# Kernel optimization log

Hardware: AMD Instinct MI355X
Metric: run time of the kernel (lower is better)

The kernel has to match this reference:

```python
import jax, jax.numpy as jnp
import numpy as np

C = 384       # in_channels
P = 64        # patch_size (H = W = P)
NH = 3        # num_heads
EPS = 1e-5
SCALE = (C // NH) ** -0.5  # head_dim in torch code = in_channels // num_heads


def _ln(x, w, b):
    m = jnp.mean(x, axis=-1, keepdims=True)
    v = jnp.var(x, axis=-1, keepdims=True)
    return (x - m) / jnp.sqrt(v + EPS) * w + b


def _dwt2d(x):
    # Haar DWT, x: [B, C, H, W] -> [B, 4C, H/2, W/2] channels = [LL, HL, LH, HH]
    x01 = x[:, :, 0::2, :] / 2
    x02 = x[:, :, 1::2, :] / 2
    x1 = x01[:, :, :, 0::2]
    x2 = x02[:, :, :, 0::2]
    x3 = x01[:, :, :, 1::2]
    x4 = x02[:, :, :, 1::2]
    return jnp.concatenate(
        [x1 + x2 + x3 + x4, -x1 - x2 + x3 + x4, -x1 + x2 - x3 + x4, x1 - x2 - x3 + x4],
        axis=1)


def _iwt2d(x):
    # inverse Haar, x: [B, 4C, h, w] -> [B, C, 2h, 2w]
    B, C4, h, w = x.shape
    c = C4 // 4
    x1 = x[:, 0:c] / 2
    x2 = x[:, c:2 * c] / 2
    x3 = x[:, 2 * c:3 * c] / 2
    x4 = x[:, 3 * c:4 * c] / 2
    out = jnp.zeros((B, c, h * 2, w * 2), x.dtype)
    out = out.at[:, :, 0::2, 0::2].set(x1 - x2 - x3 + x4)
    out = out.at[:, :, 1::2, 0::2].set(x1 - x2 + x3 - x4)
    out = out.at[:, :, 0::2, 1::2].set(x1 + x2 - x3 - x4)
    out = out.at[:, :, 1::2, 1::2].set(x1 + x2 + x3 + x4)
    return out


def setup_inputs():
    key = jax.random.key(0)
    ks = jax.random.split(key, 6)
    B, L = 8, P * P
    s = 0.02
    f32 = jnp.float32
    return {
        "sf": jax.random.normal(ks[0], (B, L, C), f32),
        "wf": jax.random.normal(ks[1], (B, L, C), f32),
        "q_w": jax.random.normal(ks[2], (C, C), f32) * s,
        "q_b": jnp.zeros((C,), f32),
        "q_ln_w": jnp.ones((C,), f32),
        "q_ln_b": jnp.zeros((C,), f32),
        "kv_w": jax.random.normal(ks[3], (2 * C, C), f32) * s,
        "kv_b": jnp.zeros((2 * C,), f32),
        "kv_ln_w": jnp.ones((2 * C,), f32),
        "kv_ln_b": jnp.zeros((2 * C,), f32),
        "out_w": jax.random.normal(ks[4], (C, C), f32) * s,
        "out_b": jnp.zeros((C,), f32),
    }


def reference(sf, wf, q_w, q_b, q_ln_w, q_ln_b, kv_w, kv_b, kv_ln_w, kv_ln_b, out_w, out_b):
    B, L, _ = sf.shape
    H = W = P
    h, w = H // 2, W // 2
    n = h * w  # L // 4

    t_sf = _ln(sf @ q_w.T + q_b, q_ln_w, q_ln_b)            # [B, L, C]
    t_wf = _ln(wf @ kv_w.T + kv_b, kv_ln_w, kv_ln_b)        # [B, L, 2C]

    t_sf = t_sf.reshape(B, H, W, C).transpose(0, 3, 1, 2)
    t_wf = t_wf.reshape(B, H, W, 2 * C).transpose(0, 3, 1, 2)

    t_sf = _dwt2d(t_sf).transpose(0, 2, 3, 1).reshape(B, n, 4 * C)
    t_wf = _dwt2d(t_wf).transpose(0, 2, 3, 1).reshape(B, n, 8 * C)

    k_all, v_all = jnp.split(t_wf, 2, axis=-1)              # each [B, n, 4C]
    q1, q2 = t_sf[..., :C], t_sf[..., C:]
    k1, k2 = k_all[..., :C], k_all[..., C:]
    v1, v2 = v_all[..., :C], v_all[..., C:]

    # branch 1: full single-head attention on LL sub-band (no scale, as in source)
    att1 = jax.nn.softmax(jnp.einsum('bnc,bmc->bnm', q1, k1), axis=-1)
    x1 = jnp.einsum('bnm,bmc->bnc', att1, v1)
    x1 = x1.reshape(B, h, w, C).transpose(0, 3, 1, 2)       # [B, C, h, w]

    # branch 2: multi-head attention on high-freq sub-bands, per-head dim = 3C/NH = C
    d = (3 * C) // NH
    q2 = q2.reshape(B, n, NH, d).transpose(0, 2, 1, 3)      # [B, NH, n, d]
    k2 = k2.reshape(B, n, NH, d).transpose(0, 2, 1, 3)
    v2 = v2.reshape(B, n, NH, d).transpose(0, 2, 3, 1)      # [B, NH, d, n]
    att2 = jax.nn.softmax(jnp.einsum('bhnd,bhmd->bhnm', q2, k2) * SCALE, axis=-1)
    x2 = jnp.einsum('bhdm,bhmn->bhdn', v2, att2)            # [B, NH, d, n]
    x2 = x2.reshape(B, NH * d, h, w)                        # [B, 3C, h, w]

    x = jnp.concatenate([x1, x2], axis=1)                   # [B, 4C, h, w]
    x = _iwt2d(x)                                           # [B, C, H, W]
    x = x.transpose(0, 2, 3, 1).reshape(B, L, C)
    return x @ out_w.T + out_b
```

## Files before the change

### kernel.cpp

```cpp
#include <hip/hip_runtime.h>
#include <hip/hip_bf16.h>

typedef unsigned short u16;
typedef unsigned int u32;
typedef __attribute__((ext_vector_type(8))) short short8;
typedef __attribute__((ext_vector_type(4))) float f32x4;

#define MFMA_BF16(A, B, C) __builtin_amdgcn_mfma_f32_16x16x32_bf16(A, B, C, 0, 0, 0)

#define SCALE2 0.08838834764831845f
#define LNEPS 1e-5f

__device__ __forceinline__ float b2f(u16 u) {
  return __uint_as_float(((u32)u) << 16);
}
__device__ __forceinline__ u16 f2b(float f) {
  u32 x = __float_as_uint(f);
  return (u16)((x + 0x7fffu + ((x >> 16) & 1u)) >> 16);
}
__device__ __forceinline__ float ldf(const float* p) { return *p; }
__device__ __forceinline__ float ldf(const u16* p) { return b2f(*p); }
__device__ __forceinline__ void stf(float* p, float v) { *p = v; }
__device__ __forceinline__ void stf(u16* p, float v) { *p = f2b(v); }

template <int SPLIT, typename TX, typename TO>
__global__ __launch_bounds__(256) void gemm_mfma(
    const TX* __restrict__ X, const float* __restrict__ W,
    const float* __restrict__ bias, TO* __restrict__ out) {
  __shared__ __align__(16) u16 AH[128 * 40];
  __shared__ __align__(16) u16 BH[128 * 40];
  __shared__ __align__(16) u16 AL[SPLIT ? 128 * 40 : 8];
  __shared__ __align__(16) u16 BL[SPLIT ? 128 * 40 : 8];
  const int tid = threadIdx.x;
  const int w = tid >> 6, lane = tid & 63;
  const int t = lane & 15, qd = lane >> 4;
  const int wm = w & 1, wn = w >> 1;
  const int m0 = blockIdx.y * 128, n0 = blockIdx.x * 128;
  f32x4 acc[4][4];
#pragma unroll
  for (int i = 0; i < 4; ++i)
#pragma unroll
    for (int j = 0; j < 4; ++j) acc[i][j] = (f32x4){0.f, 0.f, 0.f, 0.f};
  for (int kt = 0; kt < 384; kt += 32) {
#pragma unroll
    for (int rep = 0; rep < 4; ++rep) {
      int e = tid + rep * 256;
      int m = e >> 3, k4 = (e & 7) * 4;
      if constexpr (sizeof(TX) == 4) {
        float4 v = *(const float4*)(X + (size_t)(m0 + m) * 384 + kt + k4);
        u16 h0 = f2b(v.x), h1 = f2b(v.y), h2 = f2b(v.z), h3 = f2b(v.w);
        u32 hp0 = (u32)h0 | ((u32)h1 << 16), hp1 = (u32)h2 | ((u32)h3 << 16);
        *(uint2*)&AH[m * 40 + k4] = make_uint2(hp0, hp1);
        if (SPLIT) {
          u16 l0 = f2b(v.x - b2f(h0)), l1 = f2b(v.y - b2f(h1));
          u16 l2 = f2b(v.z - b2f(h2)), l3 = f2b(v.w - b2f(h3));
          *(uint2*)&AL[m * 40 + k4] =
              make_uint2((u32)l0 | ((u32)l1 << 16), (u32)l2 | ((u32)l3 << 16));
        }
      } else {
        uint2 raw = *(const uint2*)(X + (size_t)(m0 + m) * 384 + kt + k4);
        *(uint2*)&AH[m * 40 + k4] = raw;
      }
      float4 wv = *(const float4*)(W + (size_t)(n0 + m) * 384 + kt + k4);
      u16 wh0 = f2b(wv.x), wh1 = f2b(wv.y), wh2 = f2b(wv.z), wh3 = f2b(wv.w);
      *(uint2*)&BH[m * 40 + k4] =
          make_uint2((u32)wh0 | ((u32)wh1 << 16), (u32)wh2 | ((u32)wh3 << 16));
      if (SPLIT) {
        u16 wl0 = f2b(wv.x - b2f(wh0)), wl1 = f2b(wv.y - b2f(wh1));
        u16 wl2 = f2b(wv.z - b2f(wh2)), wl3 = f2b(wv.w - b2f(wh3));
        *(uint2*)&BL[m * 40 + k4] =
            make_uint2((u32)wl0 | ((u32)wl1 << 16), (u32)wl2 | ((u32)wl3 << 16));
      }
    }
    __syncthreads();
    short8 af[4], bf[4], al[4], bl[4];
#pragma unroll
    for (int mi = 0; mi < 4; ++mi) {
      af[mi] = *(const short8*)&AH[(wm * 64 + mi * 16 + t) * 40 + qd * 8];
      bf[mi] = *(const short8*)&BH[(wn * 64 + mi * 16 + t) * 40 + qd * 8];
      if (SPLIT) {
        al[mi] = *(const short8*)&AL[(wm * 64 + mi * 16 + t) * 40 + qd * 8];
        bl[mi] = *(const short8*)&BL[(wn * 64 + mi * 16 + t) * 40 + qd * 8];
      }
    }
#pragma unroll
    for (int mi = 0; mi < 4; ++mi)
#pragma unroll
      for (int ni = 0; ni < 4; ++ni) {
        acc[mi][ni] = MFMA_BF16(af[mi], bf[ni], acc[mi][ni]);
        if (SPLIT) {
          acc[mi][ni] = MFMA_BF16(al[mi], bf[ni], acc[mi][ni]);
          acc[mi][ni] = MFMA_BF16(af[mi], bl[ni], acc[mi][ni]);
        }
      }
    __syncthreads();
  }
#pragma unroll
  for (int ni = 0; ni < 4; ++ni) {
    int n = n0 + wn * 64 + ni * 16 + t;
    float bv = bias[n];
#pragma unroll
    for (int mi = 0; mi < 4; ++mi)
#pragma unroll
      for (int r = 0; r < 4; ++r) {
        int m = m0 + wm * 64 + mi * 16 + qd * 4 + r;
        stf(&out[(size_t)m * 384 + n], acc[mi][ni][r] + bv);
      }
  }
}

template <typename T>
__global__ __launch_bounds__(256) void ln_inplace(
    T* __restrict__ Tb, const float* __restrict__ w, const float* __restrict__ b, int N) {
  const int row = blockIdx.x, tid = threadIdx.x;
  T* Tr = Tb + (size_t)row * N;
  float vals[3];
  float s = 0.f, ss = 0.f;
  int nv = 0;
  for (int i = tid; i < N; i += 256) {
    float v = ldf(&Tr[i]);
    vals[nv++] = v;
    s += v; ss += v * v;
  }
#pragma unroll
  for (int mk = 32; mk; mk >>= 1) { s += __shfl_xor(s, mk); ss += __shfl_xor(ss, mk); }
  __shared__ float red[8];
  if ((tid & 63) == 0) { red[tid >> 6] = s; red[4 + (tid >> 6)] = ss; }
  __syncthreads();
  s = red[0] + red[1] + red[2] + red[3];
  ss = red[4] + red[5] + red[6] + red[7];
  float inv = 1.f / (float)N;
  float mean = s * inv;
  float var = fmaxf(ss * inv - mean * mean, 0.f);
  float rstd = rsqrtf(var + LNEPS);
  nv = 0;
  for (int i = tid; i < N; i += 256) {
    float v = (vals[nv++] - mean) * rstd * w[i] + b[i];
    stf(&Tr[i], v);
  }
}

__global__ __launch_bounds__(256) void ln_wf_split(
    float* __restrict__ lo, u16* __restrict__ hi,
    const float* __restrict__ w, const float* __restrict__ b) {
  const int row = blockIdx.x, tid = threadIdx.x;
  float* L = lo + (size_t)row * 384;
  u16* H = hi + (size_t)row * 384;
  float vals[3];
  float s = 0.f, ss = 0.f;
  int nv = 0;
  for (int i = tid; i < 768; i += 256) {
    float v = (i < 384) ? L[i] : b2f(H[i - 384]);
    vals[nv++] = v;
    s += v; ss += v * v;
  }
#pragma unroll
  for (int mk = 32; mk; mk >>= 1) { s += __shfl_xor(s, mk); ss += __shfl_xor(ss, mk); }
  __shared__ float red[8];
  if ((tid & 63) == 0) { red[tid >> 6] = s; red[4 + (tid >> 6)] = ss; }
  __syncthreads();
  s = red[0] + red[1] + red[2] + red[3];
  ss = red[4] + red[5] + red[6] + red[7];
  float mean = s * (1.f / 768.f);
  float var = fmaxf(ss * (1.f / 768.f) - mean * mean, 0.f);
  float rstd = rsqrtf(var + LNEPS);
  nv = 0;
  for (int i = 0 + tid; i < 768; i += 256) {
    float v = (vals[nv++] - mean) * rstd * w[i] + b[i];
    if (i < 384) L[i] = v; else H[i - 384] = f2b(v);
  }
}

__global__ __launch_bounds__(256) void dwt_sf(
    const float* __restrict__ T, u16* __restrict__ q1h, u16* __restrict__ q1l,
    u16* __restrict__ q2) {
  const int blk = blockIdx.x;
  const int b = blk >> 10, pos = blk & 1023;
  const int i = pos >> 5, j = pos & 31;
  const int p00 = (i * 2) * 64 + j * 2;
  const float* base = T + (size_t)b * 4096 * 384;
  for (int ch = threadIdx.x; ch < 384; ch += 256) {
    float a  = base[(size_t)p00 * 384 + ch];
    float cc = base[(size_t)(p00 + 1) * 384 + ch];
    float bb = base[(size_t)(p00 + 64) * 384 + ch];
    float dd = base[(size_t)(p00 + 65) * 384 + ch];
    float s0 = 0.5f * ( a + bb + cc + dd);
    float s1 = 0.5f * (-a - bb + cc + dd);
    float s2 = 0.5f * (-a + bb - cc + dd);
    float s3 = 0.5f * ( a - bb - cc + dd);
    size_t po = (size_t)(b * 1024 + pos) * 384 + ch;
    u16 h = f2b(s0);
    q1h[po] = h;
    q1l[po] = f2b(s0 - b2f(h));
    q2[(size_t)((b * 3 + 0) * 1024 + pos) * 384 + ch] = f2b(s1);
    q2[(size_t)((b * 3 + 1) * 1024 + pos) * 384 + ch] = f2b(s2);
    q2[(size_t)((b * 3 + 2) * 1024 + pos) * 384 + ch] = f2b(s3);
  }
}

__global__ __launch_bounds__(256) void dwt_wf_split(
    const float* __restrict__ lo, const u16* __restrict__ hi,
    u16* __restrict__ k1h, u16* __restrict__ k1l, u16* __restrict__ v1,
    u16* __restrict__ k2, u16* __restrict__ v2) {
  const int blk = blockIdx.x;
  const int b = blk >> 10, pos = blk & 1023;
  const int i = pos >> 5, j = pos & 31;
  const int p00 = (i * 2) * 64 + j * 2;
  for (int ch = threadIdx.x; ch < 768; ch += 256) {
    float a, bb, cc, dd;
    if (ch < 384) {
      const float* base = lo + (size_t)b * 4096 * 384;
      a  = base[(size_t)p00 * 384 + ch];
      cc = base[(size_t)(p00 + 1) * 384 + ch];
      bb = base[(size_t)(p00 + 64) * 384 + ch];
      dd = base[(size_t)(p00 + 65) * 384 + ch];
    } else {
      const u16* base = hi + (size_t)b * 4096 * 384;
      int c = ch - 384;
      a  = b2f(base[(size_t)p00 * 384 + c]);
      cc = b2f(base[(size_t)(p00 + 1) * 384 + c]);
      bb = b2f(base[(size_t)(p00 + 64) * 384 + c]);
      dd = b2f(base[(size_t)(p00 + 65) * 384 + c]);
    }
    float s0 = 0.5f * ( a + bb + cc + dd);
    float s1 = 0.5f * (-a - bb + cc + dd);
    float s2 = 0.5f * (-a + bb - cc + dd);
    float s3 = 0.5f * ( a - bb - cc + dd);
    if (ch < 384) {
      size_t po = (size_t)(b * 1024 + pos) * 384 + ch;
      u16 h = f2b(s0);
      k1h[po] = h;
      k1l[po] = f2b(s0 - b2f(h));
      v1[po] = f2b(s2);
      k2[(size_t)((b * 3 + 1) * 1024 + pos) * 384 + ch] = f2b(s1);
      v2[(size_t)((b * 3 + 1) * 1024 + pos) * 384 + ch] = f2b(s3);
    } else {
      int c = ch - 384;
      k2[(size_t)((b * 3 + 0) * 1024 + pos) * 384 + c] = f2b(s0);
      k2[(size_t)((b * 3 + 2) * 1024 + pos) * 384 + c] = f2b(s1);
      v2[(size_t)((b * 3 + 0) * 1024 + pos) * 384 + c] = f2b(s2);
      v2[(size_t)((b * 3 + 2) * 1024 + pos) * 384 + c] = f2b(s3);
    }
  }
}

__global__ __launch_bounds__(256) void transpose_rm(
    const u16* __restrict__ in, u16* __restrict__ out) {
  __shared__ u16 T[64][65];
  const int tid = threadIdx.x;
  const int bh = blockIdx.z, r0 = blockIdx.y * 64, c0 = blockIdx.x * 64;
  const u16* ip = in + ((size_t)bh * 1024 + r0) * 384 + c0;
  for (int i = tid; i < 2048; i += 256) {
    int r = i >> 5, c2 = i & 31;
    u32 v = *(const u32*)(ip + (size_t)r * 384 + c2 * 2);
    T[c2 * 2][r] = (u16)v;
    T[c2 * 2 + 1][r] = (u16)(v >> 16);
  }
  __syncthreads();
  u16* op = out + ((size_t)bh * 384 + c0) * 1024 + r0;
  for (int i = tid; i < 2048; i += 256) {
    int c = i >> 5, r2 = i & 31;
    u32 v = (u32)T[c][r2 * 2] | ((u32)T[c][r2 * 2 + 1] << 16);
    *(u32*)(op + (size_t)c * 1024 + r2 * 2) = v;
  }
}

__device__ __forceinline__ void xcd24v2(int L, int& bh, int& o0) {
  int s = L >> 3;
  bh = (s >> 4) * 8 + (L & 7);
  o0 = (s & 15) * 64;
}

__global__ __launch_bounds__(256) void att2_stats(
    const u16* __restrict__ q, const u16* __restrict__ k,
    float2* __restrict__ stats, float scale) {
  __shared__ __align__(16) u16 S[2][12 * 32 * 40];
  const int tid = threadIdx.x, w = tid >> 6, lane = tid & 63;
  const int t = lane & 15, qd = lane >> 4;
  int bh, o0;
  xcd24v2(blockIdx.x, bh, o0);
  short8 Ah[12];
  {
    const u16* qp = q + ((size_t)bh * 1024 + o0 + w * 16 + t) * 384 + qd * 8;
#pragma unroll
    for (int ks = 0; ks < 12; ++ks) Ah[ks] = *(const short8*)(qp + ks * 32);
  }
  float m[4] = {-1e30f, -1e30f, -1e30f, -1e30f}, l[4] = {0.f, 0.f, 0.f, 0.f};
  const u16* kb = k + (size_t)bh * 1024 * 384;
  int buf = 0;
  for (int st = 0; st < 32; ++st) {
#pragma unroll
    for (int i = 0; i < 6; ++i) {
      int u = tid + i * 256;
      int r = u / 48, c8 = u % 48;
      int ks = c8 >> 2, qq = c8 & 3;
      uint4 v = *(const uint4*)(kb + (size_t)(st * 32 + r) * 384 + c8 * 8);
      *(uint4*)&S[buf][(ks * 32 + r) * 40 + qq * 8] = v;
    }
    __syncthreads();
    f32x4 Sa0 = {0.f,0.f,0.f,0.f}, Sb0 = {0.f,0.f,0.f,0.f};
    f32x4 Sa1 = {0.f,0.f,0.f,0.f}, Sb1 = {0.f,0.f,0.f,0.f};
#pragma unroll
    for (int ks = 0; ks < 12; ks += 2) {
      short8 B00 = *(const short8*)&S[buf][(ks * 32 + t) * 40 + qd * 8];
      short8 B01 = *(const short8*)&S[buf][((ks + 1) * 32 + t) * 40 + qd * 8];
      short8 B10 = *(const short8*)&S[buf][(ks * 32 + 16 + t) * 40 + qd * 8];
      short8 B11 = *(const short8*)&S[buf][((ks + 1) * 32 + 16 + t) * 40 + qd * 8];
      Sa0 = MFMA_BF16(Ah[ks], B00, Sa0);
      Sb0 = MFMA_BF16(Ah[ks + 1], B01, Sb0);
      Sa1 = MFMA_BF16(Ah[ks], B10, Sa1);
      Sb1 = MFMA_BF16(Ah[ks + 1], B11, Sb1);
    }
#pragma unroll
    for (int r = 0; r < 4; ++r) {
      float s0 = (Sa0[r] + Sb0[r]) * scale;
      float s1 = (Sa1[r] + Sb1[r]) * scale;
      float mx = fmaxf(s0, s1);
#pragma unroll
      for (int mk = 1; mk < 16; mk <<= 1) mx = fmaxf(mx, __shfl_xor(mx, mk));
      float nm = fmaxf(m[r], mx);
      float e = __expf(s0 - nm) + __expf(s1 - nm);
#pragma unroll
      for (int mk = 1; mk < 16; mk <<= 1) e += __shfl_xor(e, mk);
      l[r] = l[r] * __expf(m[r] - nm) + e;
      m[r] = nm;
    }
    buf ^= 1;
  }
  if (t == 0) {
#pragma unroll
    for (int r = 0; r < 4; ++r)
      stats[(size_t)bh * 1024 + o0 + w * 16 + qd * 4 + r] =
          make_float2(m[r], 1.f / l[r]);
  }
}

__global__ __launch_bounds__(256, 2) void att2_accum(
    const u16* __restrict__ own, const u16* __restrict__ str,
    const u16* __restrict__ vt, const float2* __restrict__ stats,
    u16* __restrict__ xall, float scale) {
  __shared__ __align__(16) u16 SQ[12 * 32 * 40];
  __shared__ __align__(16) u16 SV[24 * 16 * 40];
  __shared__ __align__(16) u16 P[4][16 * 40];
  const int tid = threadIdx.x, w = tid >> 6, lane = tid & 63;
  const int t = lane & 15, qd = lane >> 4;
  int bh, o0;
  xcd24v2(blockIdx.x, bh, o0);
  short8 Ah[12];
  {
    const u16* op = own + ((size_t)bh * 1024 + o0 + w * 16 + t) * 384 + qd * 8;
#pragma unroll
    for (int ks = 0; ks < 12; ++ks) Ah[ks] = *(const short8*)(op + ks * 32);
  }
  f32x4 acc[24];
#pragma unroll
  for (int i = 0; i < 24; ++i) acc[i] = (f32x4){0.f, 0.f, 0.f, 0.f};
  const u16* sb = str + (size_t)bh * 1024 * 384;
  const u16* vb = vt + (size_t)bh * 384 * 1024;
  u16* Pw = &P[w][0];
  for (int st = 0; st < 32; ++st) {
    __syncthreads();
#pragma unroll
    for (int i = 0; i < 6; ++i) {
      int u = tid + i * 256;
      int r = u / 48, c8 = u % 48;
      int ks = c8 >> 2, qq = c8 & 3;
      uint4 v = *(const uint4*)(sb + (size_t)(st * 32 + r) * 384 + c8 * 8);
      *(uint4*)&SQ[(ks * 32 + r) * 40 + qq * 8] = v;
    }
#pragma unroll
    for (int i = 0; i < 6; ++i) {
      int u = tid + i * 256;
      int d = u >> 2, cq = u & 3;
      uint4 v = *(const uint4*)(vb + (size_t)d * 1024 + st * 32 + cq * 8);
      *(uint4*)&SV[d * 40 + cq * 8] = v;
    }
    float2 cs0 = stats[(size_t)bh * 1024 + st * 32 + t];
    float2 cs1 = stats[(size_t)bh * 1024 + st * 32 + 16 + t];
    __syncthreads();
    f32x4 Sa0 = {0.f,0.f,0.f,0.f}, Sb0 = {0.f,0.f,0.f,0.f};
    f32x4 Sa1 = {0.f,0.f,0.f,0.f}, Sb1 = {0.f,0.f,0.f,0.f};
#pragma unroll
    for (int ks = 0; ks < 12; ks += 2) {
      short8 B00 = *(const short8*)&SQ[(ks * 32 + t) * 40 + qd * 8];
      short8 B01 = *(const short8*)&SQ[((ks + 1) * 32 + t) * 40 + qd * 8];
      short8 B10 = *(const short8*)&SQ[(ks * 32 + 16 + t) * 40 + qd * 8];
      short8 B11 = *(const short8*)&SQ[((ks + 1) * 32 + 16 + t) * 40 + qd * 8];
      Sa0 = MFMA_BF16(Ah[ks], B00, Sa0);
      Sb0 = MFMA_BF16(Ah[ks + 1], B01, Sb0);
      Sa1 = MFMA_BF16(Ah[ks], B10, Sa1);
      Sb1 = MFMA_BF16(Ah[ks + 1], B11, Sb1);
    }
#pragma unroll
    for (int r = 0; r < 4; ++r) {
      float p0 = __expf((Sa0[r] + Sb0[r]) * scale - cs0.x) * cs0.y;
      float p1 = __expf((Sa1[r] + Sb1[r]) * scale - cs1.x) * cs1.y;
      Pw[(qd * 4 + r) * 40 + t] = f2b(p0);
      Pw[(qd * 4 + r) * 40 + 16 + t] = f2b(p1);
    }
    short8 Pa = *(const short8*)&Pw[t * 40 + qd * 8];
#pragma unroll
    for (int nj = 0; nj < 24; ++nj) {
      short8 Vf = *(const short8*)&SV[(nj * 16 + t) * 40 + qd * 8];
      acc[nj] = MFMA_BF16(Pa, Vf, acc[nj]);
    }
  }
  const int b_out = bh / 3, off = (1 + bh % 3) * 384;
#pragma unroll
  for (int nj = 0; nj < 24; ++nj)
#pragma unroll
    for (int r = 0; r < 4; ++r) {
      int row = o0 + w * 16 + qd * 4 + r;
      int d = nj * 16 + t;
      xall[((size_t)b_out * 1024 + row) * 1536 + off + d] = f2b(acc[nj][r]);
    }
}

__global__ __launch_bounds__(256, 2) void att1_fused(
    const u16* __restrict__ qh, const u16* __restrict__ ql,
    const u16* __restrict__ kh, const u16* __restrict__ kl,
    const u16* __restrict__ vt, float* __restrict__ part,
    float2* __restrict__ ml) {
  __shared__ __align__(16) u16 KH[12 * 1288];
  __shared__ __align__(16) u16 KL[12 * 1288];
  __shared__ __align__(16) u16 P[2][16 * 40];
  __shared__ float2 comb[2][2][16];
  const int tid = threadIdx.x, w = tid >> 6, lane = tid & 63;
  const int t = lane & 15, qd = lane >> 4;
  const int wr = w & 1, sh = w >> 1;
  const int bh = blockIdx.x & 7;
  const int q = blockIdx.x >> 3;
  const int o0 = (q & 31) * 32;
  const int sseg = q >> 5;
  const int sbase = sseg * 512;
  short8 Ah[12], Al[12];
  {
    const u16* qp  = qh + ((size_t)bh * 1024 + o0 + wr * 16 + t) * 384 + qd * 8;
    const u16* qp2 = ql + ((size_t)bh * 1024 + o0 + wr * 16 + t) * 384 + qd * 8;
#pragma unroll
    for (int ks = 0; ks < 12; ++ks) {
      Ah[ks] = *(const short8*)(qp + ks * 32);
      Al[ks] = *(const short8*)(qp2 + ks * 32);
    }
  }
  f32x4 acc[12];
#pragma unroll
  for (int i = 0; i < 12; ++i) acc[i] = (f32x4){0.f, 0.f, 0.f, 0.f};
  float m[4] = {-1e30f, -1e30f, -1e30f, -1e30f}, l[4] = {0.f, 0.f, 0.f, 0.f};
  const u16* khb = kh + (size_t)bh * 1024 * 384;
  const u16* klb = kl + (size_t)bh * 1024 * 384;
  const u16* vbase = vt + ((size_t)bh * 384 + sh * 192 + t) * 1024 + sbase;
#pragma unroll
  for (int i = 0; i < 6; ++i) {
    int u = tid + i * 256;
    int r = u / 48, c8 = u % 48;
    int ks = c8 >> 2, j8 = c8 & 3;
    *(uint4*)&KH[ks * 1288 + r * 40 + j8 * 8] =
        *(const uint4*)(khb + (size_t)(sbase + r) * 384 + c8 * 8);
    *(uint4*)&KL[ks * 1288 + r * 40 + j8 * 8] =
        *(const uint4*)(klb + (size_t)(sbase + r) * 384 + c8 * 8);
  }
  __syncthreads();
  for (int st = 0; st < 16; ++st) {
    short8 Vr[12];
#pragma unroll
    for (int nj = 0; nj < 12; ++nj)
      Vr[nj] = *(const short8*)(vbase + (size_t)nj * 16 * 1024 + st * 32 + qd * 8);
    f32x4 Shh = {0.f,0.f,0.f,0.f}, Slh = {0.f,0.f,0.f,0.f}, Shl = {0.f,0.f,0.f,0.f};
#pragma unroll
    for (int ks = 0; ks < 12; ++ks) {
      short8 Bh = *(const short8*)&KH[ks * 1288 + (sh * 16 + t) * 40 + qd * 8];
      short8 Bl = *(const short8*)&KL[ks * 1288 + (sh * 16 + t) * 40 + qd * 8];
      Shh = MFMA_BF16(Ah[ks], Bh, Shh);
      Slh = MFMA_BF16(Al[ks], Bh, Slh);
      Shl = MFMA_BF16(Ah[ks], Bl, Shl);
    }
    float s[4], mx[4], e[4];
#pragma unroll
    for (int r = 0; r < 4; ++r) {
      s[r] = Shh[r] + Slh[r] + Shl[r];
      float v = s[r];
#pragma unroll
      for (int mk = 1; mk < 16; mk <<= 1) v = fmaxf(v, __shfl_xor(v, mk));
      mx[r] = v;
      float ee = __expf(s[r] - v);
#pragma unroll
      for (int mk = 1; mk < 16; mk <<= 1) ee += __shfl_xor(ee, mk);
      e[r] = ee;
    }
    if (t == 0) {
#pragma unroll
      for (int r = 0; r < 4; ++r)
        comb[wr][sh][qd * 4 + r] = make_float2(mx[r], e[r]);
    }
    __syncthreads();
    if (st < 15) {
#pragma unroll
      for (int i = 0; i < 6; ++i) {
        int u = tid + i * 256;
        int r = u / 48, c8 = u % 48;
        int ks = c8 >> 2, j8 = c8 & 3;
        *(uint4*)&KH[ks * 1288 + r * 40 + j8 * 8] =
            *(const uint4*)(khb + (size_t)(sbase + (st + 1) * 32 + r) * 384 + c8 * 8);
        *(uint4*)&KL[ks * 1288 + r * 40 + j8 * 8] =
            *(const uint4*)(klb + (size_t)(sbase + (st + 1) * 32 + r) * 384 + c8 * 8);
      }
    }
#pragma unroll
    for (int r = 0; r < 4; ++r) {
      float2 c0 = comb[wr][0][qd * 4 + r];
      float2 c1 = comb[wr][1][qd * 4 + r];
      float nm = fmaxf(m[r], fmaxf(c0.x, c1.x));
      float sc = __expf(m[r] - nm);
      l[r] = l[r] * sc + c0.y * __expf(c0.x - nm) + c1.y * __expf(c1.x - nm);
      m[r] = nm;
#pragma unroll
      for (int nj = 0; nj < 12; ++nj) acc[nj][r] *= sc;
      P[wr][(qd * 4 + r) * 40 + sh * 16 + t] = f2b(__expf(s[r] - nm));
    }
    __syncthreads();
    short8 Pa = *(const short8*)&P[wr][t * 40 + qd * 8];
#pragma unroll
    for (int nj = 0; nj < 12; ++nj) acc[nj] = MFMA_BF16(Pa, Vr[nj], acc[nj]);
  }
  float* pb = part + ((size_t)(sseg * 8 + bh) * 1024 + o0 + wr * 16) * 384;
#pragma unroll
  for (int r = 0; r < 4; ++r) {
    int row = qd * 4 + r;
#pragma unroll
    for (int nj = 0; nj < 12; ++nj)
      pb[(size_t)row * 384 + sh * 192 + nj * 16 + t] = acc[nj][r];
  }
  if (sh == 0 && t == 0) {
#pragma unroll
    for (int r = 0; r < 4; ++r)
      ml[sseg * 8192 + bh * 1024 + o0 + wr * 16 + qd * 4 + r] =
          make_float2(m[r], l[r]);
  }
}

__global__ __launch_bounds__(192) void att1_merge(
    const float* __restrict__ part, const float2* __restrict__ ml,
    u16* __restrict__ xall) {
  const int rb = blockIdx.x;
  float2 a = ml[rb];
  float2 b = ml[8192 + rb];
  float M = fmaxf(a.x, b.x);
  float e0 = __expf(a.x - M), e1 = __expf(b.x - M);
  float inv = 1.f / (a.y * e0 + b.y * e1);
  const float* p0 = part + (size_t)rb * 384;
  const float* p1 = part + (size_t)(8192 + rb) * 384;
  u16* xr = xall + (size_t)rb * 1536;
  for (int ch = threadIdx.x; ch < 384; ch += 192)
    xr[ch] = f2b((p0[ch] * e0 + p1[ch] * e1) * inv);
}

__global__ __launch_bounds__(256) void iwt_y(const u16* __restrict__ xall, u16* __restrict__ y) {
  const int blk = blockIdx.x;
  const int b = blk >> 10, pos = blk & 1023;
  const int i = pos >> 5, j = pos & 31;
  const u16* xr = xall + (size_t)(b * 1024 + pos) * 1536;
  u16* yb = y + (size_t)b * 4096 * 384;
  const int p00 = (i * 2) * 64 + j * 2;
  for (int c = threadIdx.x; c < 384; c += 256) {
    float g1 = 0.5f * b2f(xr[c]);
    float g2 = 0.5f * b2f(xr[c + 384]);
    float g3 = 0.5f * b2f(xr[c + 768]);
    float g4 = 0.5f * b2f(xr[c + 1152]);
    yb[(size_t)p00 * 384 + c]        = f2b(g1 - g2 - g3 + g4);
    yb[(size_t)(p00 + 64) * 384 + c] = f2b(g1 - g2 + g3 - g4);
    yb[(size_t)(p00 + 1) * 384 + c]  = f2b(g1 + g2 - g3 - g4);
    yb[(size_t)(p00 + 65) * 384 + c] = f2b(g1 + g2 + g3 + g4);
  }
}

extern "C" void kernel_launch(void* const* d_in, const int* in_sizes, int n_in,
                              void* d_out, int out_size, void* d_ws, size_t ws_size,
                              hipStream_t stream) {
  (void)in_sizes; (void)n_in; (void)out_size; (void)ws_size;
  const float* sf      = (const float*)d_in[0];
  const float* wf      = (const float*)d_in[1];
  const float* q_w     = (const float*)d_in[2];
  const float* q_b     = (const float*)d_in[3];
  const float* q_ln_w  = (const float*)d_in[4];
  const float* q_ln_b  = (const float*)d_in[5];
  const float* kv_w    = (const float*)d_in[6];
  const float* kv_b    = (const float*)d_in[7];
  const float* kv_ln_w = (const float*)d_in[8];
  const float* kv_ln_b = (const float*)d_in[9];
  const float* out_w   = (const float*)d_in[10];
  const float* out_b   = (const float*)d_in[11];
  float* out = (float*)d_out;

  char* p = (char*)d_ws;
  float* A  = (float*)p; p += 50331648;
  float* B1 = (float*)p; p += 50331648;
  u16*   B2 = (u16*)p;   p += 25165824;
  u16* q1h = (u16*)p; p += 6291456;
  u16* q1l = (u16*)p; p += 6291456;
  u16* q2  = (u16*)p; p += 18874368;
  u16* v2  = (u16*)p; p += 18874368;
  float2* stats1 = (float2*)p; p += 65536;
  float2* stats2 = (float2*)p;
  (void)stats1;
  u16* k1h = (u16*)A;
  u16* k1l = k1h + 3145728;
  u16* v1  = k1l + 3145728;
  u16* k2  = v1 + 3145728;
  u16* v1t = k2 + 9437184;
  float2* ml1 = (float2*)((char*)A + 44040192);
  u16* xall = (u16*)B1;
  float* part1 = (float*)((char*)B1 + 25165824);
  u16* v2t = B2;
  u16* y   = B2;

  gemm_mfma<1, float, float><<<dim3(3, 256), 256, 0, stream>>>(sf, q_w, q_b, A);
  ln_inplace<float><<<32768, 256, 0, stream>>>(A, q_ln_w, q_ln_b, 384);
  gemm_mfma<1, float, float><<<dim3(3, 256), 256, 0, stream>>>(wf, kv_w, kv_b, B1);
  gemm_mfma<0, float, u16><<<dim3(3, 256), 256, 0, stream>>>(wf, kv_w + 384 * 384, kv_b + 384, B2);
  ln_wf_split<<<32768, 256, 0, stream>>>(B1, B2, kv_ln_w, kv_ln_b);

  dwt_sf<<<8192, 256, 0, stream>>>(A, q1h, q1l, q2);
  dwt_wf_split<<<8192, 256, 0, stream>>>(B1, B2, k1h, k1l, v1, k2, v2);

  transpose_rm<<<dim3(6, 16, 8), 256, 0, stream>>>(v1, v1t);
  transpose_rm<<<dim3(6, 16, 24), 256, 0, stream>>>(v2, v2t);

  att2_stats<<<384, 256, 0, stream>>>(q2, k2, stats2, SCALE2);
  att1_fused<<<512, 256, 0, stream>>>(q1h, q1l, k1h, k1l, v1t, part1, ml1);
  att1_merge<<<8192, 192, 0, stream>>>(part1, ml1, xall);
  att2_accum<<<384, 256, 0, stream>>>(k2, q2, v2t, stats2, xall, SCALE2);

  iwt_y<<<8192, 256, 0, stream>>>(xall, y);
  gemm_mfma<0, u16, float><<<dim3(3, 256), 256, 0, stream>>>(y, out_w, out_b, out);
}
```

Measured before the change: 762.2 us.

## Transpose QK MFMA so softmax row stats reduce in-lane, restructure att1 pipeline

In att2_stats and att1_fused the QK^T MFMA operands are swapped so each lane holds scores for a single query row. Row max and sum then reduce mostly within registers and need only two cross-lane shuffles instead of four-step shuffle trees per row. att1_fused no longer splits keys across wave pairs with a shared-memory combine. Each wave now processes all keys in 16-key steps with double-buffered K tiles, and it defers the max rescale to every second step so it happens once per PV MFMA. The cost is more careful exp handling: probabilities use a lagged max and could overflow if scores jump sharply between steps.

```diff
diff --git a/kernel.cpp b/kernel.cpp
--- a/kernel.cpp
+++ b/kernel.cpp
@@ -285,7 +285,7 @@
 #pragma unroll
     for (int ks = 0; ks < 12; ++ks) Ah[ks] = *(const short8*)(qp + ks * 32);
   }
-  float m[4] = {-1e30f, -1e30f, -1e30f, -1e30f}, l[4] = {0.f, 0.f, 0.f, 0.f};
+  float m = -1e30f, l = 0.f;
   const u16* kb = k + (size_t)bh * 1024 * 384;
   int buf = 0;
   for (int st = 0; st < 32; ++st) {
@@ -298,41 +298,30 @@
       *(uint4*)&S[buf][(ks * 32 + r) * 40 + qq * 8] = v;
     }
     __syncthreads();
-    f32x4 Sa0 = {0.f,0.f,0.f,0.f}, Sb0 = {0.f,0.f,0.f,0.f};
-    f32x4 Sa1 = {0.f,0.f,0.f,0.f}, Sb1 = {0.f,0.f,0.f,0.f};
-#pragma unroll
-    for (int ks = 0; ks < 12; ks += 2) {
-      short8 B00 = *(const short8*)&S[buf][(ks * 32 + t) * 40 + qd * 8];
-      short8 B01 = *(const short8*)&S[buf][((ks + 1) * 32 + t) * 40 + qd * 8];
-      short8 B10 = *(const short8*)&S[buf][(ks * 32 + 16 + t) * 40 + qd * 8];
-      short8 B11 = *(const short8*)&S[buf][((ks + 1) * 32 + 16 + t) * 40 + qd * 8];
-      Sa0 = MFMA_BF16(Ah[ks], B00, Sa0);
-      Sb0 = MFMA_BF16(Ah[ks + 1], B01, Sb0);
-      Sa1 = MFMA_BF16(Ah[ks], B10, Sa1);
-      Sb1 = MFMA_BF16(Ah[ks + 1], B11, Sb1);
-    }
-#pragma unroll
-    for (int r = 0; r < 4; ++r) {
-      float s0 = (Sa0[r] + Sb0[r]) * scale;
-      float s1 = (Sa1[r] + Sb1[r]) * scale;
-      float mx = fmaxf(s0, s1);
-#pragma unroll
-      for (int mk = 1; mk < 16; mk <<= 1) mx = fmaxf(mx, __shfl_xor(mx, mk));
-      float nm = fmaxf(m[r], mx);
-      float e = __expf(s0 - nm) + __expf(s1 - nm);
-#pragma unroll
-      for (int mk = 1; mk < 16; mk <<= 1) e += __shfl_xor(e, mk);
-      l[r] = l[r] * __expf(m[r] - nm) + e;
-      m[r] = nm;
-    }
+    f32x4 Sg0 = {0.f,0.f,0.f,0.f}, Sg1 = {0.f,0.f,0.f,0.f};
+#pragma unroll
+    for (int ks = 0; ks < 12; ++ks) {
+      short8 A0 = *(const short8*)&S[buf][(ks * 32 + t) * 40 + qd * 8];
+      short8 A1 = *(const short8*)&S[buf][(ks * 32 + 16 + t) * 40 + qd * 8];
+      Sg0 = MFMA_BF16(A0, Ah[ks], Sg0);
+      Sg1 = MFMA_BF16(A1, Ah[ks], Sg1);
+    }
+    float s0 = Sg0[0]*scale, s1 = Sg0[1]*scale, s2 = Sg0[2]*scale, s3 = Sg0[3]*scale;
+    float s4 = Sg1[0]*scale, s5 = Sg1[1]*scale, s6 = Sg1[2]*scale, s7 = Sg1[3]*scale;
+    float mx = fmaxf(fmaxf(fmaxf(s0,s1),fmaxf(s2,s3)),fmaxf(fmaxf(s4,s5),fmaxf(s6,s7)));
+    mx = fmaxf(mx, __shfl_xor(mx, 16));
+    mx = fmaxf(mx, __shfl_xor(mx, 32));
+    float nm = fmaxf(m, mx);
+    float e = __expf(s0-nm)+__expf(s1-nm)+__expf(s2-nm)+__expf(s3-nm)
+            + __expf(s4-nm)+__expf(s5-nm)+__expf(s6-nm)+__expf(s7-nm);
+    e += __shfl_xor(e, 16);
+    e += __shfl_xor(e, 32);
+    l = l * __expf(m - nm) + e;
+    m = nm;
     buf ^= 1;
   }
-  if (t == 0) {
-#pragma unroll
-    for (int r = 0; r < 4; ++r)
-      stats[(size_t)bh * 1024 + o0 + w * 16 + qd * 4 + r] =
-          make_float2(m[r], 1.f / l[r]);
-  }
+  if (qd == 0)
+    stats[(size_t)bh * 1024 + o0 + w * 16 + t] = make_float2(m, 1.f / l);
 }
 
 __global__ __launch_bounds__(256, 2) void att2_accum(
@@ -421,13 +410,12 @@
     const u16* __restrict__ kh, const u16* __restrict__ kl,
     const u16* __restrict__ vt, float* __restrict__ part,
     float2* __restrict__ ml) {
-  __shared__ __align__(16) u16 KH[12 * 1288];
-  __shared__ __align__(16) u16 KL[12 * 1288];
-  __shared__ __align__(16) u16 P[2][16 * 40];
-  __shared__ float2 comb[2][2][16];
+  __shared__ __align__(16) u16 KH[2][12 * 640];
+  __shared__ __align__(16) u16 KL[2][12 * 640];
+  __shared__ __align__(16) u16 P[4][16 * 32];
   const int tid = threadIdx.x, w = tid >> 6, lane = tid & 63;
   const int t = lane & 15, qd = lane >> 4;
-  const int wr = w & 1, sh = w >> 1;
+  const int wr = w & 1, dh = w >> 1;
   const int bh = blockIdx.x & 7;
   const int q = blockIdx.x >> 3;
   const int o0 = (q & 31) * 32;
@@ -446,82 +434,92 @@
   f32x4 acc[12];
 #pragma unroll
   for (int i = 0; i < 12; ++i) acc[i] = (f32x4){0.f, 0.f, 0.f, 0.f};
-  float m[4] = {-1e30f, -1e30f, -1e30f, -1e30f}, l[4] = {0.f, 0.f, 0.f, 0.f};
-  const u16* khb = kh + (size_t)bh * 1024 * 384;
-  const u16* klb = kl + (size_t)bh * 1024 * 384;
-  const u16* vbase = vt + ((size_t)bh * 384 + sh * 192 + t) * 1024 + sbase;
-#pragma unroll
-  for (int i = 0; i < 6; ++i) {
+  float m = 0.f, l = 0.f, mxp = -1e30f;
+  const u16* khb = kh + ((size_t)bh * 1024 + sbase) * 384;
+  const u16* klb = kl + ((size_t)bh * 1024 + sbase) * 384;
+  u16* Pw = &P[w][0];
+#pragma unroll
+  for (int i = 0; i < 3; ++i) {
     int u = tid + i * 256;
     int r = u / 48, c8 = u % 48;
     int ks = c8 >> 2, j8 = c8 & 3;
-    *(uint4*)&KH[ks * 1288 + r * 40 + j8 * 8] =
-        *(const uint4*)(khb + (size_t)(sbase + r) * 384 + c8 * 8);
-    *(uint4*)&KL[ks * 1288 + r * 40 + j8 * 8] =
-        *(const uint4*)(klb + (size_t)(sbase + r) * 384 + c8 * 8);
+    *(uint4*)&KH[0][ks * 640 + r * 40 + j8 * 8] =
+        *(const uint4*)(khb + (size_t)r * 384 + c8 * 8);
+    *(uint4*)&KL[0][ks * 640 + r * 40 + j8 * 8] =
+        *(const uint4*)(klb + (size_t)r * 384 + c8 * 8);
   }
   __syncthreads();
-  for (int st = 0; st < 16; ++st) {
-    short8 Vr[12];
-#pragma unroll
-    for (int nj = 0; nj < 12; ++nj)
-      Vr[nj] = *(const short8*)(vbase + (size_t)nj * 16 * 1024 + st * 32 + qd * 8);
-    f32x4 Shh = {0.f,0.f,0.f,0.f}, Slh = {0.f,0.f,0.f,0.f}, Shl = {0.f,0.f,0.f,0.f};
-#pragma unroll
-    for (int ks = 0; ks < 12; ++ks) {
-      short8 Bh = *(const short8*)&KH[ks * 1288 + (sh * 16 + t) * 40 + qd * 8];
-      short8 Bl = *(const short8*)&KL[ks * 1288 + (sh * 16 + t) * 40 + qd * 8];
-      Shh = MFMA_BF16(Ah[ks], Bh, Shh);
-      Slh = MFMA_BF16(Al[ks], Bh, Slh);
-      Shl = MFMA_BF16(Ah[ks], Bl, Shl);
-    }
-    float s[4], mx[4], e[4];
-#pragma unroll
-    for (int r = 0; r < 4; ++r) {
-      s[r] = Shh[r] + Slh[r] + Shl[r];
-      float v = s[r];
-#pragma unroll
-      for (int mk = 1; mk < 16; mk <<= 1) v = fmaxf(v, __shfl_xor(v, mk));
-      mx[r] = v;
-      float ee = __expf(s[r] - v);
-#pragma unroll
-      for (int mk = 1; mk < 16; mk <<= 1) ee += __shfl_xor(ee, mk);
-      e[r] = ee;
-    }
-    if (t == 0) {
-#pragma unroll
-      for (int r = 0; r < 4; ++r)
-        comb[wr][sh][qd * 4 + r] = make_float2(mx[r], e[r]);
-    }
-    __syncthreads();
-    if (st < 15) {
-#pragma unroll
-      for (int i = 0; i < 6; ++i) {
+  short8 Vr[12];
+  for (int st = 0; st < 32; ++st) {
+    const int buf = st & 1;
+    if (!(st & 1)) {
+#pragma unroll
+      for (int nj = 0; nj < 12; ++nj)
+        Vr[nj] = *(const short8*)(vt +
+            ((size_t)bh * 384 + dh * 192 + nj * 16 + t) * 1024 +
+            sbase + st * 16 + qd * 8);
+    }
+    if (st < 31) {
+      const int nb = buf ^ 1;
+      const u16* kh2 = khb + (size_t)(st + 1) * 16 * 384;
+      const u16* kl2 = klb + (size_t)(st + 1) * 16 * 384;
+#pragma unroll
+      for (int i = 0; i < 3; ++i) {
         int u = tid + i * 256;
         int r = u / 48, c8 = u % 48;
         int ks = c8 >> 2, j8 = c8 & 3;
-        *(uint4*)&KH[ks * 1288 + r * 40 + j8 * 8] =
-            *(const uint4*)(khb + (size_t)(sbase + (st + 1) * 32 + r) * 384 + c8 * 8);
-        *(uint4*)&KL[ks * 1288 + r * 40 + j8 * 8] =
-            *(const uint4*)(klb + (size_t)(sbase + (st + 1) * 32 + r) * 384 + c8 * 8);
+        *(uint4*)&KH[nb][ks * 640 + r * 40 + j8 * 8] =
+            *(const uint4*)(kh2 + (size_t)r * 384 + c8 * 8);
+        *(uint4*)&KL[nb][ks * 640 + r * 40 + j8 * 8] =
+            *(const uint4*)(kl2 + (size_t)r * 384 + c8 * 8);
       }
     }
-#pragma unroll
-    for (int r = 0; r < 4; ++r) {
-      float2 c0 = comb[wr][0][qd * 4 + r];
-      float2 c1 = comb[wr][1][qd * 4 + r];
-      float nm = fmaxf(m[r], fmaxf(c0.x, c1.x));
-      float sc = __expf(m[r] - nm);
-      l[r] = l[r] * sc + c0.y * __expf(c0.x - nm) + c1.y * __expf(c1.x - nm);
-      m[r] = nm;
-#pragma unroll
-      for (int nj = 0; nj < 12; ++nj) acc[nj][r] *= sc;
-      P[wr][(qd * 4 + r) * 40 + sh * 16 + t] = f2b(__expf(s[r] - nm));
+    f32x4 Shh = {0.f,0.f,0.f,0.f}, Slh = {0.f,0.f,0.f,0.f}, Shl = {0.f,0.f,0.f,0.f};
+#pragma unroll
+    for (int ks = 0; ks < 12; ++ks) {
+      short8 Bh = *(const short8*)&KH[buf][ks * 640 + t * 40 + qd * 8];
+      short8 Bl = *(const short8*)&KL[buf][ks * 640 + t * 40 + qd * 8];
+      Shh = MFMA_BF16(Bh, Ah[ks], Shh);
+      Slh = MFMA_BF16(Bh, Al[ks], Slh);
+      Shl = MFMA_BF16(Bl, Ah[ks], Shl);
+    }
+    float s0 = Shh[0] + Slh[0] + Shl[0];
+    float s1 = Shh[1] + Slh[1] + Shl[1];
+    float s2 = Shh[2] + Slh[2] + Shl[2];
+    float s3 = Shh[3] + Slh[3] + Shl[3];
+    float mx = fmaxf(fmaxf(s0, s1), fmaxf(s2, s3));
+    mx = fmaxf(mx, __shfl_xor(mx, 16));
+    mx = fmaxf(mx, __shfl_xor(mx, 32));
+    if (st == 0) m = mx;
+    mxp = fmaxf(mxp, mx);
+    float p0 = __expf(s0 - m), p1 = __expf(s1 - m);
+    float p2 = __expf(s2 - m), p3 = __expf(s3 - m);
+    float e = p0 + p1 + p2 + p3;
+    e += __shfl_xor(e, 16);
+    e += __shfl_xor(e, 32);
+    l += e;
+    Pw[t * 32 + buf * 16 + qd * 4 + 0] = f2b(p0);
+    Pw[t * 32 + buf * 16 + qd * 4 + 1] = f2b(p1);
+    Pw[t * 32 + buf * 16 + qd * 4 + 2] = f2b(p2);
+    Pw[t * 32 + buf * 16 + qd * 4 + 3] = f2b(p3);
+    if (st & 1) {
+      short8 Pa = *(const short8*)&Pw[t * 32 + qd * 8];
+#pragma unroll
+      for (int nj = 0; nj < 12; ++nj) acc[nj] = MFMA_BF16(Pa, Vr[nj], acc[nj]);
+      float mnew = fmaxf(m, mxp);
+      float sc = __expf(m - mnew);
+      l *= sc; m = mnew; mxp = -1e30f;
+      float f0 = __shfl(sc, qd * 4 + 0);
+      float f1 = __shfl(sc, qd * 4 + 1);
+      float f2v = __shfl(sc, qd * 4 + 2);
+      float f3 = __shfl(sc, qd * 4 + 3);
+#pragma unroll
+      for (int nj = 0; nj < 12; ++nj) {
+        acc[nj][0] *= f0; acc[nj][1] *= f1;
+        acc[nj][2] *= f2v; acc[nj][3] *= f3;
+      }
     }
     __syncthreads();
-    short8 Pa = *(const short8*)&P[wr][t * 40 + qd * 8];
-#pragma unroll
-    for (int nj = 0; nj < 12; ++nj) acc[nj] = MFMA_BF16(Pa, Vr[nj], acc[nj]);
   }
   float* pb = part + ((size_t)(sseg * 8 + bh) * 1024 + o0 + wr * 16) * 384;
 #pragma unroll
@@ -529,14 +527,10 @@
     int row = qd * 4 + r;
 #pragma unroll
     for (int nj = 0; nj < 12; ++nj)
-      pb[(size_t)row * 384 + sh * 192 + nj * 16 + t] = acc[nj][r];
-  }
-  if (sh == 0 && t == 0) {
-#pragma unroll
-    for (int r = 0; r < 4; ++r)
-      ml[sseg * 8192 + bh * 1024 + o0 + wr * 16 + qd * 4 + r] =
-          make_float2(m[r], l[r]);
-  }
+      pb[(size_t)row * 384 + dh * 192 + nj * 16 + t] = acc[nj][r];
+  }
+  if (dh == 0 && qd == 0)
+    ml[sseg * 8192 + bh * 1024 + o0 + wr * 16 + t] = make_float2(m, l);
 }
 
 __global__ __launch_bounds__(192) void att1_merge(
```

Measured after the change: 738.6 us. 1.03x faster.
